# Kernel optimization log

Measured on AMD Instinct MI355X. Metric: run time of the kernel, lower is better.

The kernel has to match this reference:

```python
import jax, jax.numpy as jnp
import numpy as np

C_IMG, C_TXT, NHEAD = 256, 768, 8
B, D, H, W, L = 8, 24, 24, 24, 77

def setup_inputs() -> dict:
    key = jax.random.key(0)
    ks = jax.random.split(key, 16)
    s = 0.02
    x_img = jax.random.normal(ks[0], (B, C_IMG, D, H, W), jnp.float32)
    x_txt = jax.random.normal(ks[1], (B, L, C_TXT), jnp.float32)
    # realistic padding: each sample has a valid length in [40, 77); True = padded key
    lengths = jax.random.randint(ks[2], (B,), 40, L)
    txt_mask = jnp.arange(L)[None, :] >= lengths[:, None]  # [B, L] bool
    inp = {
        "x_img": x_img,
        "x_txt": x_txt,
        "txt_mask": txt_mask,
        "q_proj_w": jax.random.normal(ks[3], (C_IMG, C_IMG), jnp.float32) * s,   # Conv3d 1x1, no bias
        "k_proj_w": jax.random.normal(ks[4], (C_IMG, C_TXT), jnp.float32) * s,   # Linear, no bias
        "v_proj_w": jax.random.normal(ks[5], (C_IMG, C_TXT), jnp.float32) * s,
        "in_q_w": jax.random.normal(ks[6], (C_IMG, C_IMG), jnp.float32) * s,     # MHA in_proj (q/k/v)
        "in_q_b": jnp.zeros((C_IMG,), jnp.float32),
        "in_k_w": jax.random.normal(ks[7], (C_IMG, C_IMG), jnp.float32) * s,
        "in_k_b": jnp.zeros((C_IMG,), jnp.float32),
        "in_v_w": jax.random.normal(ks[8], (C_IMG, C_IMG), jnp.float32) * s,
        "in_v_b": jnp.zeros((C_IMG,), jnp.float32),
        "out_proj_w": jax.random.normal(ks[9], (C_IMG, C_IMG), jnp.float32) * s, # MHA out_proj
        "out_proj_b": jnp.zeros((C_IMG,), jnp.float32),
        "out_conv_w": jax.random.normal(ks[10], (C_IMG, C_IMG), jnp.float32) * s, # self.out Conv3d 1x1 (bias)
        "out_conv_b": jnp.zeros((C_IMG,), jnp.float32),
        "norm_w": jnp.ones((C_IMG,), jnp.float32),  # InstanceNorm3d affine
        "norm_b": jnp.zeros((C_IMG,), jnp.float32),
    }
    return inp

def reference(x_img, x_txt, txt_mask, q_proj_w, k_proj_w, v_proj_w,
              in_q_w, in_q_b, in_k_w, in_k_b, in_v_w, in_v_b,
              out_proj_w, out_proj_b, out_conv_w, out_conv_b, norm_w, norm_b):
    Bq, C, d, h, w = x_img.shape
    N = d * h * w
    hd = C // NHEAD
    # q_proj (1x1 conv == channel matmul), flatten to tokens
    q = jnp.einsum('bcdhw,oc->bodhw', x_img, q_proj_w).reshape(Bq, C, N).transpose(0, 2, 1)  # [B,N,C]
    k = jnp.einsum('blt,ct->blc', x_txt, k_proj_w)  # [B,L,C]
    v = jnp.einsum('blt,ct->blc', x_txt, v_proj_w)
    # MHA internal projections
    qh = (q @ in_q_w.T + in_q_b).reshape(Bq, N, NHEAD, hd).transpose(0, 2, 1, 3)  # [B,h,N,hd]
    kh = (k @ in_k_w.T + in_k_b).reshape(Bq, -1, NHEAD, hd).transpose(0, 2, 1, 3)  # [B,h,L,hd]
    vh = (v @ in_v_w.T + in_v_b).reshape(Bq, -1, NHEAD, hd).transpose(0, 2, 1, 3)
    scores = jnp.einsum('bhnd,bhld->bhnl', qh, kh) / jnp.sqrt(jnp.asarray(hd, qh.dtype))
    neg = jnp.finfo(scores.dtype).min
    scores = jnp.where(txt_mask[:, None, None, :], neg, scores)
    attn = jax.nn.softmax(scores, axis=-1)  # [B,h,N,L]
    o = jnp.einsum('bhnl,bhld->bhnd', attn, vh).transpose(0, 2, 1, 3).reshape(Bq, N, C)
    o = o @ out_proj_w.T + out_proj_b
    o = o.transpose(0, 2, 1).reshape(Bq, C, d, h, w)
    # self.out 1x1 conv with bias
    o = jnp.einsum('bcdhw,oc->bodhw', o, out_conv_w) + out_conv_b[None, :, None, None, None]
    # residual + InstanceNorm3d(affine) + SiLU
    r = o + x_img
    mu = r.mean(axis=(2, 3, 4), keepdims=True)
    var = r.var(axis=(2, 3, 4), keepdims=True)
    xn = (r - mu) * jax.lax.rsqrt(var + 1e-5)
    out = jax.nn.silu(xn * norm_w[None, :, None, None, None] + norm_b[None, :, None, None, None])
    return out
```

## Files before the change

### kernel.cpp

```cpp
#include <hip/hip_runtime.h>
#include <cstdint>
#include <cstddef>

#define B_    8
#define CI    256
#define NH    8
#define HD    32
#define LQ    77
#define LP    80
#define NSP   13824
#define NTILE 216
#define SCALE 0.17677669529663687f

typedef float    float4_ __attribute__((ext_vector_type(4)));
typedef _Float16 half4_  __attribute__((ext_vector_type(4)));

#define MFMA16(a,b,c) __builtin_amdgcn_mfma_f32_16x16x16f16((a),(b),(c),0,0,0)

#define OFF_WK   0
#define OFF_WV   (OFF_WK + 256*768)
#define OFF_BO   (OFF_WV + 256*768)
#define OFF_IQBS (OFF_BO + 256)
#define OFF_AM   (OFF_IQBS + 256)
#define OFF_WQP  (OFF_AM + B_*LP)
#define OFF_WOP  (OFF_WQP + 32768)
#define OFF_KP   (OFF_WOP + 32768)
#define OFF_VP   (OFF_KP + 81920)

__global__ __launch_bounds__(256) void prep_kernel(
    const float* __restrict__ qpw, const float* __restrict__ iqw,
    const float* __restrict__ opw, const float* __restrict__ opb,
    const float* __restrict__ ocw, const float* __restrict__ ocb,
    const float* __restrict__ kpw, const float* __restrict__ ikw,
    const float* __restrict__ vpw, const float* __restrict__ ivw,
    const float* __restrict__ iqb,
    const void*  __restrict__ mask_in, float* __restrict__ ws)
{
    int blk = blockIdx.x, tid = threadIdx.x;
    if (blk < 512) {
        __shared__ float col[256];
        int cc = blk & 255;
        bool isQ = blk < 256;
        const float* pw = isQ ? qpw : opw;
        const float* iw = isQ ? iqw : ocw;
        col[tid] = pw[tid * 256 + cc];
        __syncthreads();
        const float* row = iw + tid * 256;
        float a = 0.f;
        #pragma unroll 4
        for (int m = 0; m < 256; ++m) a = fmaf(row[m], col[m], a);
        if (isQ) a *= SCALE;
        _Float16* dst = (_Float16*)(ws + (isQ ? OFF_WQP : OFF_WOP));
        int kt = cc >> 4, ot = tid >> 4;
        int lane = (tid & 15) + 16 * ((cc >> 2) & 3);
        dst[((kt * 16 + ot) * 64 + lane) * 4 + (cc & 3)] = (_Float16)a;
    } else if (blk == 512) {
        float a = ocb[tid];
        const float* row = ocw + tid * 256;
        #pragma unroll 4
        for (int m = 0; m < 256; ++m) a = fmaf(row[m], opb[m], a);
        ws[OFF_BO + tid] = a;
        ws[OFF_IQBS + tid] = iqb[tid] * SCALE;
    } else if (blk < 513 + 2 * 768) {
        int j = blk - 513;
        bool isK = j < 768;
        if (!isK) j -= 768;
        int flat = j * 256 + tid;
        int o = flat / 768, tt = flat % 768;
        const float* iw = isK ? ikw : ivw;
        const float* pw = isK ? kpw : vpw;
        const float* row = iw + o * 256;
        float a = 0.f;
        #pragma unroll 4
        for (int m = 0; m < 256; ++m) a = fmaf(row[m], pw[m * 768 + tt], a);
        ws[(isK ? OFF_WK : OFF_WV) + flat] = a;
    } else {
        __shared__ int s_is8;
        if (tid == 0) s_is8 = 0;
        __syncthreads();
        const unsigned char* m8 = (const unsigned char*)mask_in;
        for (int i = tid; i < B_ * LQ; i += 256)
            if ((i & 3) && m8[i]) atomicExch(&s_is8, 1);
        __syncthreads();
        int is8 = s_is8;
        const int* mi = (const int*)mask_in;
        float* mo = ws + OFF_AM;
        for (int i = tid; i < B_ * LP; i += 256) {
            int b = i / LP, l = i % LP;
            int v = 1;
            if (l < LQ) v = is8 ? (int)m8[b * LQ + l] : mi[b * LQ + l];
            mo[i] = v ? -1e30f : 0.0f;
        }
    }
}

__global__ __launch_bounds__(256) void kv_kernel(
    const float* __restrict__ xtxt, float* __restrict__ ws,
    const float* __restrict__ ikb, const float* __restrict__ ivb)
{
    const float* Wk = ws + OFF_WK;
    const float* Wv = ws + OFF_WV;
    _Float16* kp = (_Float16*)(ws + OFF_KP);
    _Float16* vp = (_Float16*)(ws + OFF_VP);

    int b = blockIdx.y;
    int l0 = blockIdx.x * 8;
    int lcnt = (LQ - l0 < 8) ? (LQ - l0) : 8;
    __shared__ float xr[8][768];
    for (int idx = threadIdx.x; idx < 8 * 768; idx += 256) {
        int j = idx / 768, tt = idx % 768;
        xr[j][tt] = (j < lcnt) ? xtxt[((size_t)(b * LQ + l0 + j)) * 768 + tt] : 0.f;
    }
    __syncthreads();
    int o = threadIdx.x;
    float ak[8], av[8];
    #pragma unroll
    for (int j = 0; j < 8; ++j) { ak[j] = ikb[o]; av[j] = ivb[o]; }
    const float* wkr = Wk + (size_t)o * 768;
    const float* wvr = Wv + (size_t)o * 768;
    for (int tt = 0; tt < 768; ++tt) {
        float wk = wkr[tt], wv = wvr[tt];
        #pragma unroll
        for (int j = 0; j < 8; ++j) {
            ak[j] = fmaf(wk, xr[j][tt], ak[j]);
            av[j] = fmaf(wv, xr[j][tt], av[j]);
        }
    }
    int h = o >> 5, d = o & 31;
    size_t hb = (size_t)(b * NH + h);
    #pragma unroll
    for (int j = 0; j < 8; ++j) {
        if (j < lcnt) {
            int l = l0 + j;
            int lt = l >> 4;
            kp[(hb * 10 + lt * 2 + (d >> 4)) * 256 +
               ((l & 15) + 16 * ((d >> 2) & 3)) * 4 + (d & 3)] = (_Float16)ak[j];
            vp[(hb * 10 + (d >> 4) * 5 + lt) * 256 +
               ((d & 15) + 16 * ((l & 15) >> 2)) * 4 + (l & 3)] = (_Float16)av[j];
        }
    }
}

__global__ __launch_bounds__(256, 2) void main_kernel(
    const float* __restrict__ x_img, const float* __restrict__ ws,
    float* __restrict__ rout)
{
    const _Float16* wqpk = (const _Float16*)(ws + OFF_WQP);
    const _Float16* wopk = (const _Float16*)(ws + OFF_WOP);
    const _Float16* kpck = (const _Float16*)(ws + OFF_KP);
    const _Float16* vpck = (const _Float16*)(ws + OFF_VP);
    const float* iqbs = ws + OFF_IQBS;
    const float* bog  = ws + OFF_BO;

    __shared__ _Float16 sh0[16384];
    __shared__ _Float16 qls[16384];
    __shared__ float am_s[LP];

    const int tid  = threadIdx.x;
    const int lane = tid & 63;
    const int w    = __builtin_amdgcn_readfirstlane(tid >> 6);
    const int g    = lane >> 4;
    const int li   = lane & 15;
    const int by   = blockIdx.y;
    const int n0   = blockIdx.x * 64;

    const float* xba = x_img + (size_t)by * CI * NSP + n0;
    float*       rba = rout  + (size_t)by * CI * NSP + n0;

    if (tid < LP) am_s[tid] = ws[OFF_AM + by * LP + tid];

    for (int it = 0; it < 8; ++it) {
        int idx = it * 256 + tid;
        int c = idx >> 3, hl = idx & 7;
        const float* gp = xba + (size_t)c * NSP + hl * 8;
        float4_ a = *(const float4_*)gp;
        float4_ bvv = *(const float4_*)(gp + 4);
        int kt = c >> 4;
        int lhi = 16 * ((c >> 2) & 3);
        int jj = c & 3;
        #pragma unroll
        for (int u = 0; u < 8; ++u) {
            int t = hl * 8 + u;
            float v = (u < 4) ? a[u] : bvv[u - 4];
            sh0[((kt * 4 + (t >> 4)) * 64 + (t & 15) + lhi) * 4 + jj] = (_Float16)v;
        }
    }
    __syncthreads();

    float4_ acc[4][4];
    #pragma unroll
    for (int of = 0; of < 4; ++of) {
        float bs[4];
        #pragma unroll
        for (int r = 0; r < 4; ++r) bs[r] = iqbs[w * 64 + of * 16 + 4 * g + r];
        #pragma unroll
        for (int tf = 0; tf < 4; ++tf)
            #pragma unroll
            for (int r = 0; r < 4; ++r) acc[of][tf][r] = bs[r];
    }
    for (int kt = 0; kt < 16; ++kt) {
        half4_ bfr[4], afr[4];
        #pragma unroll
        for (int tf = 0; tf < 4; ++tf)
            bfr[tf] = *(const half4_*)&sh0[((kt * 4 + tf) * 64 + lane) * 4];
        #pragma unroll
        for (int of = 0; of < 4; ++of)
            afr[of] = *(const half4_*)&wqpk[((kt * 16 + w * 4 + of) * 64 + lane) * 4];
        #pragma unroll
        for (int of = 0; of < 4; ++of)
            #pragma unroll
            for (int tf = 0; tf < 4; ++tf)
                acc[of][tf] = MFMA16(afr[of], bfr[tf], acc[of][tf]);
    }
    #pragma unroll
    for (int of = 0; of < 4; ++of)
        #pragma unroll
        for (int tf = 0; tf < 4; ++tf) {
            half4_ qv;
            #pragma unroll
            for (int r = 0; r < 4; ++r) qv[r] = (_Float16)acc[of][tf][r];
            *(half4_*)&qls[((( w * 4 + of) * 4 + tf) * 64 + lane) * 4] = qv;
        }
    __syncthreads();

    for (int hh = 0; hh < 2; ++hh) {
        const int h = 2 * w + hh;
        half4_ qb[2][4];
        #pragma unroll
        for (int kd = 0; kd < 2; ++kd)
            #pragma unroll
            for (int tf = 0; tf < 4; ++tf)
                qb[kd][tf] = *(const half4_*)&qls[(((h * 2 + kd) * 4 + tf) * 64 + lane) * 4];
        float4_ sc[5][4];
        #pragma unroll
        for (int lt = 0; lt < 5; ++lt)
            #pragma unroll
            for (int tf = 0; tf < 4; ++tf)
                #pragma unroll
                for (int r = 0; r < 4; ++r) sc[lt][tf][r] = 0.f;
        const _Float16* kp = kpck + (size_t)(by * NH + h) * 10 * 256;
        #pragma unroll
        for (int lt = 0; lt < 5; ++lt)
            #pragma unroll
            for (int kd = 0; kd < 2; ++kd) {
                half4_ akf = *(const half4_*)&kp[((lt * 2 + kd) * 64 + lane) * 4];
                #pragma unroll
                for (int tf = 0; tf < 4; ++tf)
                    sc[lt][tf] = MFMA16(akf, qb[kd][tf], sc[lt][tf]);
            }
        float mk[5][4];
        #pragma unroll
        for (int lt = 0; lt < 5; ++lt)
            #pragma unroll
            for (int r = 0; r < 4; ++r) mk[lt][r] = am_s[lt * 16 + 4 * g + r];
        #pragma unroll
        for (int lt = 0; lt < 5; ++lt)
            #pragma unroll
            for (int tf = 0; tf < 4; ++tf)
                #pragma unroll
                for (int r = 0; r < 4; ++r) sc[lt][tf][r] += mk[lt][r];
        float mx[4], sm[4], inv[4];
        #pragma unroll
        for (int tf = 0; tf < 4; ++tf) {
            float m = -3.0e38f;
            #pragma unroll
            for (int lt = 0; lt < 5; ++lt)
                #pragma unroll
                for (int r = 0; r < 4; ++r) m = fmaxf(m, sc[lt][tf][r]);
            m = fmaxf(m, __shfl_xor(m, 16));
            m = fmaxf(m, __shfl_xor(m, 32));
            mx[tf] = m;
        }
        #pragma unroll
        for (int tf = 0; tf < 4; ++tf) {
            float s = 0.f;
            #pragma unroll
            for (int lt = 0; lt < 5; ++lt)
                #pragma unroll
                for (int r = 0; r < 4; ++r) {
                    float e = __expf(sc[lt][tf][r] - mx[tf]);
                    sc[lt][tf][r] = e;
                    s += e;
                }
            s += __shfl_xor(s, 16);
            s += __shfl_xor(s, 32);
            sm[tf] = s;
            inv[tf] = 1.0f / s;
        }
        float4_ oa[2][4];
        #pragma unroll
        for (int dt = 0; dt < 2; ++dt)
            #pragma unroll
            for (int tf = 0; tf < 4; ++tf)
                #pragma unroll
                for (int r = 0; r < 4; ++r) oa[dt][tf][r] = 0.f;
        const _Float16* vp = vpck + (size_t)(by * NH + h) * 10 * 256;
        #pragma unroll
        for (int lt = 0; lt < 5; ++lt) {
            half4_ pl[4];
            #pragma unroll
            for (int tf = 0; tf < 4; ++tf) {
                #pragma unroll
                for (int r = 0; r < 4; ++r) pl[tf][r] = (_Float16)sc[lt][tf][r];
            }
            #pragma unroll
            for (int dt = 0; dt < 2; ++dt) {
                half4_ avf = *(const half4_*)&vp[((dt * 5 + lt) * 64 + lane) * 4];
                #pragma unroll
                for (int tf = 0; tf < 4; ++tf)
                    oa[dt][tf] = MFMA16(avf, pl[tf], oa[dt][tf]);
            }
        }
        #pragma unroll
        for (int dt = 0; dt < 2; ++dt)
            #pragma unroll
            for (int tf = 0; tf < 4; ++tf) {
                half4_ ov;
                #pragma unroll
                for (int r = 0; r < 4; ++r) ov[r] = (_Float16)(oa[dt][tf][r] * inv[tf]);
                *(half4_*)&sh0[(((h * 2 + dt) * 4 + tf) * 64 + lane) * 4] = ov;
            }
    }
    __syncthreads();

    float4_ fa[4][4];
    #pragma unroll
    for (int of = 0; of < 4; ++of) {
        float bs[4];
        #pragma unroll
        for (int r = 0; r < 4; ++r) bs[r] = bog[w * 64 + of * 16 + 4 * g + r];
        #pragma unroll
        for (int tf = 0; tf < 4; ++tf)
            #pragma unroll
            for (int r = 0; r < 4; ++r) fa[of][tf][r] = bs[r];
    }
    for (int kt = 0; kt < 16; ++kt) {
        half4_ bfr[4], afr[4];
        #pragma unroll
        for (int tf = 0; tf < 4; ++tf)
            bfr[tf] = *(const half4_*)&sh0[((kt * 4 + tf) * 64 + lane) * 4];
        #pragma unroll
        for (int of = 0; of < 4; ++of)
            afr[of] = *(const half4_*)&wopk[((kt * 16 + w * 4 + of) * 64 + lane) * 4];
        #pragma unroll
        for (int of = 0; of < 4; ++of)
            #pragma unroll
            for (int tf = 0; tf < 4; ++tf)
                fa[of][tf] = MFMA16(afr[of], bfr[tf], fa[of][tf]);
    }
    #pragma unroll
    for (int of = 0; of < 4; ++of)
        #pragma unroll
        for (int tf = 0; tf < 4; ++tf)
            #pragma unroll
            for (int r = 0; r < 4; ++r) {
                int o = w * 64 + of * 16 + 4 * g + r;
                int t = tf * 16 + li;
                size_t a = (size_t)o * NSP + t;
                rba[a] = fa[of][tf][r] + xba[a];
            }
}

__global__ __launch_bounds__(256) void norm_kernel(
    float* __restrict__ rout, const float* __restrict__ nw, const float* __restrict__ nb)
{
    __shared__ float red[8];
    __shared__ float stats[2];
    int blk = blockIdx.x;
    int c = blk & 255;
    float* row = rout + (size_t)blk * NSP;
    float4_* row4 = (float4_*)row;
    int tid = threadIdx.x;

    float s = 0.f, s2 = 0.f;
    for (int i = tid; i < NSP / 4; i += 256) {
        float4_ v = row4[i];
        #pragma unroll
        for (int u = 0; u < 4; ++u) { s += v[u]; s2 = fmaf(v[u], v[u], s2); }
    }
    #pragma unroll
    for (int off = 32; off > 0; off >>= 1) {
        s  += __shfl_down(s, off);
        s2 += __shfl_down(s2, off);
    }
    int wv = tid >> 6, ln = tid & 63;
    if (ln == 0) { red[wv] = s; red[4 + wv] = s2; }
    __syncthreads();
    if (tid == 0) {
        float S  = red[0] + red[1] + red[2] + red[3];
        float S2 = red[4] + red[5] + red[6] + red[7];
        float mu = S / (float)NSP;
        float var = S2 / (float)NSP - mu * mu;
        stats[0] = mu;
        stats[1] = rsqrtf(var + 1e-5f);
    }
    __syncthreads();
    float mu = stats[0], rstd = stats[1];
    float gg  = nw[c] * rstd;
    float b2 = fmaf(-mu, gg, nb[c]);
    for (int i = tid; i < NSP / 4; i += 256) {
        float4_ v = row4[i];
        #pragma unroll
        for (int u = 0; u < 4; ++u) {
            float y = fmaf(v[u], gg, b2);
            v[u] = y / (1.f + __expf(-y));
        }
        row4[i] = v;
    }
}

extern "C" void kernel_launch(void* const* d_in, const int* in_sizes, int n_in,
                              void* d_out, int out_size, void* d_ws, size_t ws_size,
                              hipStream_t stream) {
    const float* x_img = (const float*)d_in[0];
    const float* x_txt = (const float*)d_in[1];
    const void*  tmask = d_in[2];
    const float* qpw   = (const float*)d_in[3];
    const float* kpw   = (const float*)d_in[4];
    const float* vpw   = (const float*)d_in[5];
    const float* iqw   = (const float*)d_in[6];
    const float* iqb   = (const float*)d_in[7];
    const float* ikw   = (const float*)d_in[8];
    const float* ikb   = (const float*)d_in[9];
    const float* ivw   = (const float*)d_in[10];
    const float* ivb   = (const float*)d_in[11];
    const float* opw   = (const float*)d_in[12];
    const float* opb   = (const float*)d_in[13];
    const float* ocw   = (const float*)d_in[14];
    const float* ocb   = (const float*)d_in[15];
    const float* nw    = (const float*)d_in[16];
    const float* nb    = (const float*)d_in[17];
    float* ws  = (float*)d_ws;
    float* out = (float*)d_out;

    prep_kernel<<<2050, 256, 0, stream>>>(qpw, iqw, opw, opb, ocw, ocb,
                                          kpw, ikw, vpw, ivw, iqb, tmask, ws);
    kv_kernel<<<dim3(10, B_), 256, 0, stream>>>(x_txt, ws, ikb, ivb);
    main_kernel<<<dim3(NTILE, B_), 256, 0, stream>>>(x_img, ws, out);
    norm_kernel<<<B_ * CI, 256, 0, stream>>>(out, nw, nb);
}
```

Baseline: 513.5 us.

## Move weight combining and KV projection to MFMA, fuse norm stats into main kernel

The scalar weight-combination and K/V projection kernels are replaced with MFMA-based fp16 versions that write directly into the packed fragment layouts. The main kernel drops the second shared buffer to raise occupancy to 3 blocks per CU. It also stages its output through swizzled shared memory for coalesced stores and accumulates per-channel sum and sum-of-squares with atomics. The norm kernel then only reads the precomputed stats and does a single pass over the data instead of two. The cost is extra fp16 rounding of weights and inputs, plus atomic contention on the statistics buffer.

```diff
diff --git a/kernel.cpp b/kernel.cpp
--- a/kernel.cpp
+++ b/kernel.cpp
@@ -17,64 +17,31 @@
 
 #define MFMA16(a,b,c) __builtin_amdgcn_mfma_f32_16x16x16f16((a),(b),(c),0,0,0)
 
-#define OFF_WK   0
-#define OFF_WV   (OFF_WK + 256*768)
-#define OFF_BO   (OFF_WV + 256*768)
-#define OFF_IQBS (OFF_BO + 256)
-#define OFF_AM   (OFF_IQBS + 256)
-#define OFF_WQP  (OFF_AM + B_*LP)
-#define OFF_WOP  (OFF_WQP + 32768)
-#define OFF_KP   (OFF_WOP + 32768)
-#define OFF_VP   (OFF_KP + 81920)
+#define OFF_WQP  0
+#define OFF_WOP  32768
+#define OFF_WKP  65536
+#define OFF_WVP  163840
+#define OFF_KP   262144
+#define OFF_VP   344064
+#define OFF_BO   425984
+#define OFF_IQBS 426240
+#define OFF_AM   426496
+#define OFF_STAT 427136
 
 __global__ __launch_bounds__(256) void prep_kernel(
-    const float* __restrict__ qpw, const float* __restrict__ iqw,
-    const float* __restrict__ opw, const float* __restrict__ opb,
-    const float* __restrict__ ocw, const float* __restrict__ ocb,
-    const float* __restrict__ kpw, const float* __restrict__ ikw,
-    const float* __restrict__ vpw, const float* __restrict__ ivw,
-    const float* __restrict__ iqb,
+    const float* __restrict__ opb, const float* __restrict__ ocw,
+    const float* __restrict__ ocb, const float* __restrict__ iqb,
     const void*  __restrict__ mask_in, float* __restrict__ ws)
 {
     int blk = blockIdx.x, tid = threadIdx.x;
-    if (blk < 512) {
-        __shared__ float col[256];
-        int cc = blk & 255;
-        bool isQ = blk < 256;
-        const float* pw = isQ ? qpw : opw;
-        const float* iw = isQ ? iqw : ocw;
-        col[tid] = pw[tid * 256 + cc];
-        __syncthreads();
-        const float* row = iw + tid * 256;
-        float a = 0.f;
-        #pragma unroll 4
-        for (int m = 0; m < 256; ++m) a = fmaf(row[m], col[m], a);
-        if (isQ) a *= SCALE;
-        _Float16* dst = (_Float16*)(ws + (isQ ? OFF_WQP : OFF_WOP));
-        int kt = cc >> 4, ot = tid >> 4;
-        int lane = (tid & 15) + 16 * ((cc >> 2) & 3);
-        dst[((kt * 16 + ot) * 64 + lane) * 4 + (cc & 3)] = (_Float16)a;
-    } else if (blk == 512) {
+    if (blk == 0) {
         float a = ocb[tid];
         const float* row = ocw + tid * 256;
         #pragma unroll 4
         for (int m = 0; m < 256; ++m) a = fmaf(row[m], opb[m], a);
         ws[OFF_BO + tid] = a;
         ws[OFF_IQBS + tid] = iqb[tid] * SCALE;
-    } else if (blk < 513 + 2 * 768) {
-        int j = blk - 513;
-        bool isK = j < 768;
-        if (!isK) j -= 768;
-        int flat = j * 256 + tid;
-        int o = flat / 768, tt = flat % 768;
-        const float* iw = isK ? ikw : ivw;
-        const float* pw = isK ? kpw : vpw;
-        const float* row = iw + o * 256;
-        float a = 0.f;
-        #pragma unroll 4
-        for (int m = 0; m < 256; ++m) a = fmaf(row[m], pw[m * 768 + tt], a);
-        ws[(isK ? OFF_WK : OFF_WV) + flat] = a;
-    } else {
+    } else if (blk == 1) {
         __shared__ int s_is8;
         if (tid == 0) s_is8 = 0;
         __syncthreads();
@@ -91,6 +58,67 @@
             if (l < LQ) v = is8 ? (int)m8[b * LQ + l] : mi[b * LQ + l];
             mo[i] = v ? -1e30f : 0.0f;
         }
+    } else {
+        for (int i = tid; i < B_ * CI * 2; i += 256) ws[OFF_STAT + i] = 0.f;
+    }
+}
+
+__global__ __launch_bounds__(256) void wcomb_kernel(
+    const float* __restrict__ qpw, const float* __restrict__ iqw,
+    const float* __restrict__ opw, const float* __restrict__ ocw,
+    const float* __restrict__ kpw, const float* __restrict__ ikw,
+    const float* __restrict__ vpw, const float* __restrict__ ivw,
+    float* __restrict__ ws)
+{
+    int blk = blockIdx.x, tid = threadIdx.x;
+    int lane = tid & 63, w = tid >> 6, g = lane >> 4, li = lane & 15;
+
+    const float *iw, *pw; _Float16* dst; int pstride, ctb, otb; float scale = 1.f;
+    if (blk < 16) {
+        iw = iqw; pw = qpw; pstride = 256; dst = (_Float16*)(ws + OFF_WQP);
+        ctb = blk >> 2; otb = blk & 3; scale = SCALE;
+    } else if (blk < 32) {
+        int j = blk - 16;
+        iw = ocw; pw = opw; pstride = 256; dst = (_Float16*)(ws + OFF_WOP);
+        ctb = j >> 2; otb = j & 3;
+    } else if (blk < 80) {
+        int j = blk - 32;
+        iw = ikw; pw = kpw; pstride = 768; dst = (_Float16*)(ws + OFF_WKP);
+        ctb = j >> 2; otb = j & 3;
+    } else {
+        int j = blk - 80;
+        iw = ivw; pw = vpw; pstride = 768; dst = (_Float16*)(ws + OFF_WVP);
+        ctb = j >> 2; otb = j & 3;
+    }
+    int ct = ctb * 4 + w;
+
+    float4_ acc[4];
+    #pragma unroll
+    for (int i = 0; i < 4; ++i)
+        #pragma unroll
+        for (int r = 0; r < 4; ++r) acc[i][r] = 0.f;
+
+    for (int mt = 0; mt < 16; ++mt) {
+        half4_ ah;
+        #pragma unroll
+        for (int j = 0; j < 4; ++j)
+            ah[j] = (_Float16)pw[(size_t)(mt * 16 + 4 * g + j) * pstride + ct * 16 + li];
+        #pragma unroll
+        for (int i = 0; i < 4; ++i) {
+            int o = (otb * 4 + i) * 16 + li;
+            float4_ bw = *(const float4_*)&iw[(size_t)o * 256 + mt * 16 + 4 * g];
+            half4_ bh;
+            #pragma unroll
+            for (int j = 0; j < 4; ++j) bh[j] = (_Float16)bw[j];
+            acc[i] = MFMA16(ah, bh, acc[i]);
+        }
+    }
+    #pragma unroll
+    for (int i = 0; i < 4; ++i) {
+        half4_ oh;
+        #pragma unroll
+        for (int r = 0; r < 4; ++r) oh[r] = (_Float16)(acc[i][r] * scale);
+        *(half4_*)&dst[((size_t)(ct * 16 + otb * 4 + i) * 64 + lane) * 4] = oh;
     }
 }
 
@@ -98,52 +126,86 @@
     const float* __restrict__ xtxt, float* __restrict__ ws,
     const float* __restrict__ ikb, const float* __restrict__ ivb)
 {
-    const float* Wk = ws + OFF_WK;
-    const float* Wv = ws + OFF_WV;
+    const _Float16* wkA = (const _Float16*)(ws + OFF_WKP);
+    const _Float16* wvA = (const _Float16*)(ws + OFF_WVP);
     _Float16* kp = (_Float16*)(ws + OFF_KP);
     _Float16* vp = (_Float16*)(ws + OFF_VP);
 
-    int b = blockIdx.y;
-    int l0 = blockIdx.x * 8;
-    int lcnt = (LQ - l0 < 8) ? (LQ - l0) : 8;
-    __shared__ float xr[8][768];
-    for (int idx = threadIdx.x; idx < 8 * 768; idx += 256) {
-        int j = idx / 768, tt = idx % 768;
-        xr[j][tt] = (j < lcnt) ? xtxt[((size_t)(b * LQ + l0 + j)) * 768 + tt] : 0.f;
-    }
-    __syncthreads();
-    int o = threadIdx.x;
-    float ak[8], av[8];
-    #pragma unroll
-    for (int j = 0; j < 8; ++j) { ak[j] = ikb[o]; av[j] = ivb[o]; }
-    const float* wkr = Wk + (size_t)o * 768;
-    const float* wvr = Wv + (size_t)o * 768;
-    for (int tt = 0; tt < 768; ++tt) {
-        float wk = wkr[tt], wv = wvr[tt];
-        #pragma unroll
-        for (int j = 0; j < 8; ++j) {
-            ak[j] = fmaf(wk, xr[j][tt], ak[j]);
-            av[j] = fmaf(wv, xr[j][tt], av[j]);
-        }
-    }
-    int h = o >> 5, d = o & 31;
-    size_t hb = (size_t)(b * NH + h);
-    #pragma unroll
-    for (int j = 0; j < 8; ++j) {
-        if (j < lcnt) {
-            int l = l0 + j;
-            int lt = l >> 4;
-            kp[(hb * 10 + lt * 2 + (d >> 4)) * 256 +
-               ((l & 15) + 16 * ((d >> 2) & 3)) * 4 + (d & 3)] = (_Float16)ak[j];
-            vp[(hb * 10 + (d >> 4) * 5 + lt) * 256 +
-               ((d & 15) + 16 * ((l & 15) >> 2)) * 4 + (l & 3)] = (_Float16)av[j];
-        }
-    }
-}
-
-__global__ __launch_bounds__(256, 2) void main_kernel(
+    int b = blockIdx.x >> 1, part = blockIdx.x & 1;
+    int tid = threadIdx.x, lane = tid & 63, w = tid >> 6, g = lane >> 4, li = lane & 15;
+
+    float4_ acc[4][5];
+    if (part == 0) {
+        #pragma unroll
+        for (int i = 0; i < 4; ++i) {
+            float4_ bias = *(const float4_*)&ikb[(w * 4 + i) * 16 + 4 * g];
+            #pragma unroll
+            for (int lt = 0; lt < 5; ++lt) acc[i][lt] = bias;
+        }
+    } else {
+        #pragma unroll
+        for (int i = 0; i < 4; ++i) {
+            float bv = ivb[(w * 4 + i) * 16 + li];
+            #pragma unroll
+            for (int lt = 0; lt < 5; ++lt)
+                #pragma unroll
+                for (int r = 0; r < 4; ++r) acc[i][lt][r] = bv;
+        }
+    }
+
+    for (int kt = 0; kt < 48; ++kt) {
+        half4_ xh[5];
+        #pragma unroll
+        for (int lt = 0; lt < 5; ++lt) {
+            int l = lt * 16 + li;
+            float4_ xv = {0.f, 0.f, 0.f, 0.f};
+            if (l < LQ)
+                xv = *(const float4_*)&xtxt[(size_t)(b * LQ + l) * 768 + kt * 16 + 4 * g];
+            #pragma unroll
+            for (int j = 0; j < 4; ++j) xh[lt][j] = (_Float16)xv[j];
+        }
+        if (part == 0) {
+            #pragma unroll
+            for (int i = 0; i < 4; ++i) {
+                half4_ aw = *(const half4_*)&wkA[((size_t)(kt * 16 + w * 4 + i) * 64 + lane) * 4];
+                #pragma unroll
+                for (int lt = 0; lt < 5; ++lt)
+                    acc[i][lt] = MFMA16(aw, xh[lt], acc[i][lt]);
+            }
+        } else {
+            #pragma unroll
+            for (int i = 0; i < 4; ++i) {
+                half4_ bw = *(const half4_*)&wvA[((size_t)(kt * 16 + w * 4 + i) * 64 + lane) * 4];
+                #pragma unroll
+                for (int lt = 0; lt < 5; ++lt)
+                    acc[i][lt] = MFMA16(xh[lt], bw, acc[i][lt]);
+            }
+        }
+    }
+
+    #pragma unroll
+    for (int i = 0; i < 4; ++i) {
+        int ot = w * 4 + i, h = ot >> 1;
+        size_t hb = (size_t)(b * NH + h) * 10;
+        #pragma unroll
+        for (int lt = 0; lt < 5; ++lt) {
+            half4_ oh;
+            #pragma unroll
+            for (int r = 0; r < 4; ++r) oh[r] = (_Float16)acc[i][lt][r];
+            if (part == 0) {
+                int kd = ot & 1;
+                *(half4_*)&kp[(hb + lt * 2 + kd) * 256 + lane * 4] = oh;
+            } else {
+                int dt = ot & 1;
+                *(half4_*)&vp[(hb + dt * 5 + lt) * 256 + lane * 4] = oh;
+            }
+        }
+    }
+}
+
+__global__ __launch_bounds__(256, 3) void main_kernel(
     const float* __restrict__ x_img, const float* __restrict__ ws,
-    float* __restrict__ rout)
+    float* __restrict__ rout, float* __restrict__ stat)
 {
     const _Float16* wqpk = (const _Float16*)(ws + OFF_WQP);
     const _Float16* wopk = (const _Float16*)(ws + OFF_WOP);
@@ -153,7 +215,6 @@
     const float* bog  = ws + OFF_BO;
 
     __shared__ _Float16 sh0[16384];
-    __shared__ _Float16 qls[16384];
     __shared__ float am_s[LP];
 
     const int tid  = threadIdx.x;
@@ -169,34 +230,150 @@
 
     if (tid < LP) am_s[tid] = ws[OFF_AM + by * LP + tid];
 
-    for (int it = 0; it < 8; ++it) {
-        int idx = it * 256 + tid;
-        int c = idx >> 3, hl = idx & 7;
-        const float* gp = xba + (size_t)c * NSP + hl * 8;
-        float4_ a = *(const float4_*)gp;
-        float4_ bvv = *(const float4_*)(gp + 4);
-        int kt = c >> 4;
-        int lhi = 16 * ((c >> 2) & 3);
-        int jj = c & 3;
-        #pragma unroll
-        for (int u = 0; u < 8; ++u) {
-            int t = hl * 8 + u;
-            float v = (u < 4) ? a[u] : bvv[u - 4];
-            sh0[((kt * 4 + (t >> 4)) * 64 + (t & 15) + lhi) * 4 + jj] = (_Float16)v;
+    {
+        int t = tid & 63, tf_s = t >> 4, tl = t & 15;
+        for (int it = 0; it < 16; ++it) {
+            int cbase = it * 16 + 4 * w;
+            half4_ hv;
+            #pragma unroll
+            for (int j = 0; j < 4; ++j)
+                hv[j] = (_Float16)xba[(size_t)(cbase + j) * NSP + t];
+            *(half4_*)&sh0[((it * 4 + tf_s) * 64 + tl + 16 * w) * 4] = hv;
         }
     }
     __syncthreads();
 
-    float4_ acc[4][4];
+    half4_ qh_h[4][4];
+    {
+        float4_ acc[4][4];
+        #pragma unroll
+        for (int of = 0; of < 4; ++of) {
+            float4_ bias = *(const float4_*)&iqbs[w * 64 + of * 16 + 4 * g];
+            #pragma unroll
+            for (int tf = 0; tf < 4; ++tf) acc[of][tf] = bias;
+        }
+        for (int kt = 0; kt < 16; ++kt) {
+            half4_ bfr[4], afr[4];
+            #pragma unroll
+            for (int tf = 0; tf < 4; ++tf)
+                bfr[tf] = *(const half4_*)&sh0[((kt * 4 + tf) * 64 + lane) * 4];
+            #pragma unroll
+            for (int of = 0; of < 4; ++of)
+                afr[of] = *(const half4_*)&wqpk[((size_t)(kt * 16 + w * 4 + of) * 64 + lane) * 4];
+            #pragma unroll
+            for (int of = 0; of < 4; ++of)
+                #pragma unroll
+                for (int tf = 0; tf < 4; ++tf)
+                    acc[of][tf] = MFMA16(afr[of], bfr[tf], acc[of][tf]);
+        }
+        #pragma unroll
+        for (int of = 0; of < 4; ++of)
+            #pragma unroll
+            for (int tf = 0; tf < 4; ++tf)
+                #pragma unroll
+                for (int r = 0; r < 4; ++r)
+                    qh_h[of][tf][r] = (_Float16)acc[of][tf][r];
+    }
+    __syncthreads();
+
+    #pragma unroll
+    for (int hh = 0; hh < 2; ++hh) {
+        const int h = 2 * w + hh;
+        const _Float16* kp = kpck + (size_t)(by * NH + h) * 2560;
+        const _Float16* vp = vpck + (size_t)(by * NH + h) * 2560;
+        float mk[5][4];
+        #pragma unroll
+        for (int lt = 0; lt < 5; ++lt)
+            #pragma unroll
+            for (int r = 0; r < 4; ++r) mk[lt][r] = am_s[lt * 16 + 4 * g + r];
+        #pragma unroll
+        for (int tfh = 0; tfh < 2; ++tfh) {
+            float4_ sc[5][2];
+            #pragma unroll
+            for (int lt = 0; lt < 5; ++lt)
+                #pragma unroll
+                for (int t2 = 0; t2 < 2; ++t2)
+                    #pragma unroll
+                    for (int r = 0; r < 4; ++r) sc[lt][t2][r] = 0.f;
+            #pragma unroll
+            for (int lt = 0; lt < 5; ++lt)
+                #pragma unroll
+                for (int kd = 0; kd < 2; ++kd) {
+                    half4_ akf = *(const half4_*)&kp[((lt * 2 + kd) * 64 + lane) * 4];
+                    #pragma unroll
+                    for (int t2 = 0; t2 < 2; ++t2)
+                        sc[lt][t2] = MFMA16(akf, qh_h[2 * hh + kd][tfh * 2 + t2], sc[lt][t2]);
+                }
+            #pragma unroll
+            for (int lt = 0; lt < 5; ++lt)
+                #pragma unroll
+                for (int t2 = 0; t2 < 2; ++t2)
+                    #pragma unroll
+                    for (int r = 0; r < 4; ++r) sc[lt][t2][r] += mk[lt][r];
+            float inv[2];
+            #pragma unroll
+            for (int t2 = 0; t2 < 2; ++t2) {
+                float m = -3.0e38f;
+                #pragma unroll
+                for (int lt = 0; lt < 5; ++lt)
+                    #pragma unroll
+                    for (int r = 0; r < 4; ++r) m = fmaxf(m, sc[lt][t2][r]);
+                m = fmaxf(m, __shfl_xor(m, 16));
+                m = fmaxf(m, __shfl_xor(m, 32));
+                float s = 0.f;
+                #pragma unroll
+                for (int lt = 0; lt < 5; ++lt)
+                    #pragma unroll
+                    for (int r = 0; r < 4; ++r) {
+                        float e = __expf(sc[lt][t2][r] - m);
+                        sc[lt][t2][r] = e;
+                        s += e;
+                    }
+                s += __shfl_xor(s, 16);
+                s += __shfl_xor(s, 32);
+                inv[t2] = 1.0f / s;
+            }
+            float4_ oa[2][2];
+            #pragma unroll
+            for (int dt = 0; dt < 2; ++dt)
+                #pragma unroll
+                for (int t2 = 0; t2 < 2; ++t2)
+                    #pragma unroll
+                    for (int r = 0; r < 4; ++r) oa[dt][t2][r] = 0.f;
+            #pragma unroll
+            for (int lt = 0; lt < 5; ++lt) {
+                half4_ pl[2];
+                #pragma unroll
+                for (int t2 = 0; t2 < 2; ++t2)
+                    #pragma unroll
+                    for (int r = 0; r < 4; ++r) pl[t2][r] = (_Float16)sc[lt][t2][r];
+                #pragma unroll
+                for (int dt = 0; dt < 2; ++dt) {
+                    half4_ avf = *(const half4_*)&vp[((dt * 5 + lt) * 64 + lane) * 4];
+                    #pragma unroll
+                    for (int t2 = 0; t2 < 2; ++t2)
+                        oa[dt][t2] = MFMA16(avf, pl[t2], oa[dt][t2]);
+                }
+            }
+            #pragma unroll
+            for (int dt = 0; dt < 2; ++dt)
+                #pragma unroll
+                for (int t2 = 0; t2 < 2; ++t2) {
+                    half4_ ov;
+                    #pragma unroll
+                    for (int r = 0; r < 4; ++r) ov[r] = (_Float16)(oa[dt][t2][r] * inv[t2]);
+                    *(half4_*)&sh0[(((h * 2 + dt) * 4 + tfh * 2 + t2) * 64 + lane) * 4] = ov;
+                }
+        }
+    }
+    __syncthreads();
+
+    float4_ fa[4][4];
     #pragma unroll
     for (int of = 0; of < 4; ++of) {
-        float bs[4];
-        #pragma unroll
-        for (int r = 0; r < 4; ++r) bs[r] = iqbs[w * 64 + of * 16 + 4 * g + r];
-        #pragma unroll
-        for (int tf = 0; tf < 4; ++tf)
-            #pragma unroll
-            for (int r = 0; r < 4; ++r) acc[of][tf][r] = bs[r];
+        float4_ bias = *(const float4_*)&bog[w * 64 + of * 16 + 4 * g];
+        #pragma unroll
+        for (int tf = 0; tf < 4; ++tf) fa[of][tf] = bias;
     }
     for (int kt = 0; kt < 16; ++kt) {
         half4_ bfr[4], afr[4];
@@ -205,200 +382,69 @@
             bfr[tf] = *(const half4_*)&sh0[((kt * 4 + tf) * 64 + lane) * 4];
         #pragma unroll
         for (int of = 0; of < 4; ++of)
-            afr[of] = *(const half4_*)&wqpk[((kt * 16 + w * 4 + of) * 64 + lane) * 4];
-        #pragma unroll
-        for (int of = 0; of < 4; ++of)
-            #pragma unroll
-            for (int tf = 0; tf < 4; ++tf)
-                acc[of][tf] = MFMA16(afr[of], bfr[tf], acc[of][tf]);
-    }
-    #pragma unroll
-    for (int of = 0; of < 4; ++of)
-        #pragma unroll
-        for (int tf = 0; tf < 4; ++tf) {
-            half4_ qv;
-            #pragma unroll
-            for (int r = 0; r < 4; ++r) qv[r] = (_Float16)acc[of][tf][r];
-            *(half4_*)&qls[((( w * 4 + of) * 4 + tf) * 64 + lane) * 4] = qv;
-        }
-    __syncthreads();
-
-    for (int hh = 0; hh < 2; ++hh) {
-        const int h = 2 * w + hh;
-        half4_ qb[2][4];
-        #pragma unroll
-        for (int kd = 0; kd < 2; ++kd)
-            #pragma unroll
-            for (int tf = 0; tf < 4; ++tf)
-                qb[kd][tf] = *(const half4_*)&qls[(((h * 2 + kd) * 4 + tf) * 64 + lane) * 4];
-        float4_ sc[5][4];
-        #pragma unroll
-        for (int lt = 0; lt < 5; ++lt)
-            #pragma unroll
-            for (int tf = 0; tf < 4; ++tf)
-                #pragma unroll
-                for (int r = 0; r < 4; ++r) sc[lt][tf][r] = 0.f;
-        const _Float16* kp = kpck + (size_t)(by * NH + h) * 10 * 256;
-        #pragma unroll
-        for (int lt = 0; lt < 5; ++lt)
-            #pragma unroll
-            for (int kd = 0; kd < 2; ++kd) {
-                half4_ akf = *(const half4_*)&kp[((lt * 2 + kd) * 64 + lane) * 4];
-                #pragma unroll
-                for (int tf = 0; tf < 4; ++tf)
-                    sc[lt][tf] = MFMA16(akf, qb[kd][tf], sc[lt][tf]);
-            }
-        float mk[5][4];
-        #pragma unroll
-        for (int lt = 0; lt < 5; ++lt)
-            #pragma unroll
-            for (int r = 0; r < 4; ++r) mk[lt][r] = am_s[lt * 16 + 4 * g + r];
-        #pragma unroll
-        for (int lt = 0; lt < 5; ++lt)
-            #pragma unroll
-            for (int tf = 0; tf < 4; ++tf)
-                #pragma unroll
-                for (int r = 0; r < 4; ++r) sc[lt][tf][r] += mk[lt][r];
-        float mx[4], sm[4], inv[4];
-        #pragma unroll
-        for (int tf = 0; tf < 4; ++tf) {
-            float m = -3.0e38f;
-            #pragma unroll
-            for (int lt = 0; lt < 5; ++lt)
-                #pragma unroll
-                for (int r = 0; r < 4; ++r) m = fmaxf(m, sc[lt][tf][r]);
-            m = fmaxf(m, __shfl_xor(m, 16));
-            m = fmaxf(m, __shfl_xor(m, 32));
-            mx[tf] = m;
-        }
-        #pragma unroll
-        for (int tf = 0; tf < 4; ++tf) {
-            float s = 0.f;
-            #pragma unroll
-            for (int lt = 0; lt < 5; ++lt)
-                #pragma unroll
-                for (int r = 0; r < 4; ++r) {
-                    float e = __expf(sc[lt][tf][r] - mx[tf]);
-                    sc[lt][tf][r] = e;
-                    s += e;
-                }
-            s += __shfl_xor(s, 16);
-            s += __shfl_xor(s, 32);
-            sm[tf] = s;
-            inv[tf] = 1.0f / s;
-        }
-        float4_ oa[2][4];
-        #pragma unroll
-        for (int dt = 0; dt < 2; ++dt)
-            #pragma unroll
-            for (int tf = 0; tf < 4; ++tf)
-                #pragma unroll
-                for (int r = 0; r < 4; ++r) oa[dt][tf][r] = 0.f;
-        const _Float16* vp = vpck + (size_t)(by * NH + h) * 10 * 256;
-        #pragma unroll
-        for (int lt = 0; lt < 5; ++lt) {
-            half4_ pl[4];
-            #pragma unroll
-            for (int tf = 0; tf < 4; ++tf) {
-                #pragma unroll
-                for (int r = 0; r < 4; ++r) pl[tf][r] = (_Float16)sc[lt][tf][r];
-            }
-            #pragma unroll
-            for (int dt = 0; dt < 2; ++dt) {
-                half4_ avf = *(const half4_*)&vp[((dt * 5 + lt) * 64 + lane) * 4];
-                #pragma unroll
-                for (int tf = 0; tf < 4; ++tf)
-                    oa[dt][tf] = MFMA16(avf, pl[tf], oa[dt][tf]);
-            }
-        }
-        #pragma unroll
-        for (int dt = 0; dt < 2; ++dt)
-            #pragma unroll
-            for (int tf = 0; tf < 4; ++tf) {
-                half4_ ov;
-                #pragma unroll
-                for (int r = 0; r < 4; ++r) ov[r] = (_Float16)(oa[dt][tf][r] * inv[tf]);
-                *(half4_*)&sh0[(((h * 2 + dt) * 4 + tf) * 64 + lane) * 4] = ov;
-            }
-    }
-    __syncthreads();
-
-    float4_ fa[4][4];
-    #pragma unroll
-    for (int of = 0; of < 4; ++of) {
-        float bs[4];
-        #pragma unroll
-        for (int r = 0; r < 4; ++r) bs[r] = bog[w * 64 + of * 16 + 4 * g + r];
-        #pragma unroll
-        for (int tf = 0; tf < 4; ++tf)
-            #pragma unroll
-            for (int r = 0; r < 4; ++r) fa[of][tf][r] = bs[r];
-    }
-    for (int kt = 0; kt < 16; ++kt) {
-        half4_ bfr[4], afr[4];
-        #pragma unroll
-        for (int tf = 0; tf < 4; ++tf)
-            bfr[tf] = *(const half4_*)&sh0[((kt * 4 + tf) * 64 + lane) * 4];
-        #pragma unroll
-        for (int of = 0; of < 4; ++of)
-            afr[of] = *(const half4_*)&wopk[((kt * 16 + w * 4 + of) * 64 + lane) * 4];
+            afr[of] = *(const half4_*)&wopk[((size_t)(kt * 16 + w * 4 + of) * 64 + lane) * 4];
         #pragma unroll
         for (int of = 0; of < 4; ++of)
             #pragma unroll
             for (int tf = 0; tf < 4; ++tf)
                 fa[of][tf] = MFMA16(afr[of], bfr[tf], fa[of][tf]);
     }
+    __syncthreads();
+
     #pragma unroll
     for (int of = 0; of < 4; ++of)
         #pragma unroll
         for (int tf = 0; tf < 4; ++tf)
             #pragma unroll
             for (int r = 0; r < 4; ++r) {
-                int o = w * 64 + of * 16 + 4 * g + r;
-                int t = tf * 16 + li;
-                size_t a = (size_t)o * NSP + t;
-                rba[a] = fa[of][tf][r] + xba[a];
-            }
+                int row = w * 64 + of * 16 + 4 * g + r;
+                int q   = tf * 4 + (li >> 2);
+                int qs  = q ^ (4 * g + r);
+                sh0[row * 64 + qs * 4 + (li & 3)] = (_Float16)fa[of][tf][r];
+            }
+    __syncthreads();
+
+    for (int it = 0; it < 16; ++it) {
+        int flat = it * 256 + tid;
+        int row = flat >> 4, q = flat & 15;
+        half4_ hv = *(const half4_*)&sh0[row * 64 + ((q ^ (row & 15)) << 2)];
+        float4_ xres = *(const float4_*)&xba[(size_t)row * NSP + q * 4];
+        float4_ y;
+        float s = 0.f, s2 = 0.f;
+        #pragma unroll
+        for (int e = 0; e < 4; ++e) {
+            y[e] = (float)hv[e] + xres[e];
+            s += y[e];
+            s2 = fmaf(y[e], y[e], s2);
+        }
+        *(float4_*)&rba[(size_t)row * NSP + q * 4] = y;
+        #pragma unroll
+        for (int off = 1; off < 16; off <<= 1) {
+            s  += __shfl_xor(s, off);
+            s2 += __shfl_xor(s2, off);
+        }
+        if ((tid & 15) == 0) {
+            atomicAdd(&stat[(by * CI + row) * 2],     s);
+            atomicAdd(&stat[(by * CI + row) * 2 + 1], s2);
+        }
+    }
 }
 
 __global__ __launch_bounds__(256) void norm_kernel(
-    float* __restrict__ rout, const float* __restrict__ nw, const float* __restrict__ nb)
+    float* __restrict__ rout, const float* __restrict__ nw,
+    const float* __restrict__ nb, const float* __restrict__ stat)
 {
-    __shared__ float red[8];
-    __shared__ float stats[2];
     int blk = blockIdx.x;
     int c = blk & 255;
-    float* row = rout + (size_t)blk * NSP;
-    float4_* row4 = (float4_*)row;
-    int tid = threadIdx.x;
-
-    float s = 0.f, s2 = 0.f;
-    for (int i = tid; i < NSP / 4; i += 256) {
-        float4_ v = row4[i];
-        #pragma unroll
-        for (int u = 0; u < 4; ++u) { s += v[u]; s2 = fmaf(v[u], v[u], s2); }
-    }
-    #pragma unroll
-    for (int off = 32; off > 0; off >>= 1) {
-        s  += __shfl_down(s, off);
-        s2 += __shfl_down(s2, off);
-    }
-    int wv = tid >> 6, ln = tid & 63;
-    if (ln == 0) { red[wv] = s; red[4 + wv] = s2; }
-    __syncthreads();
-    if (tid == 0) {
-        float S  = red[0] + red[1] + red[2] + red[3];
-        float S2 = red[4] + red[5] + red[6] + red[7];
-        float mu = S / (float)NSP;
-        float var = S2 / (float)NSP - mu * mu;
-        stats[0] = mu;
-        stats[1] = rsqrtf(var + 1e-5f);
-    }
-    __syncthreads();
-    float mu = stats[0], rstd = stats[1];
-    float gg  = nw[c] * rstd;
+    float S  = stat[blk * 2];
+    float S2 = stat[blk * 2 + 1];
+    float mu = S * (1.0f / (float)NSP);
+    float var = S2 * (1.0f / (float)NSP) - mu * mu;
+    float rstd = rsqrtf(var + 1e-5f);
+    float gg = nw[c] * rstd;
     float b2 = fmaf(-mu, gg, nb[c]);
-    for (int i = tid; i < NSP / 4; i += 256) {
+    float4_* row4 = (float4_*)(rout + (size_t)blk * NSP);
+    for (int i = threadIdx.x; i < NSP / 4; i += 256) {
         float4_ v = row4[i];
         #pragma unroll
         for (int u = 0; u < 4; ++u) {
@@ -433,9 +479,9 @@
     float* ws  = (float*)d_ws;
     float* out = (float*)d_out;
 
-    prep_kernel<<<2050, 256, 0, stream>>>(qpw, iqw, opw, opb, ocw, ocb,
-                                          kpw, ikw, vpw, ivw, iqb, tmask, ws);
-    kv_kernel<<<dim3(10, B_), 256, 0, stream>>>(x_txt, ws, ikb, ivb);
-    main_kernel<<<dim3(NTILE, B_), 256, 0, stream>>>(x_img, ws, out);
-    norm_kernel<<<B_ * CI, 256, 0, stream>>>(out, nw, nb);
-}
+    prep_kernel<<<3, 256, 0, stream>>>(opb, ocw, ocb, iqb, tmask, ws);
+    wcomb_kernel<<<128, 256, 0, stream>>>(qpw, iqw, opw, ocw, kpw, ikw, vpw, ivw, ws);
+    kv_kernel<<<16, 256, 0, stream>>>(x_txt, ws, ikb, ivb);
+    main_kernel<<<dim3(NTILE, B_), 256, 0, stream>>>(x_img, ws, out, ws + OFF_STAT);
+    norm_kernel<<<B_ * CI, 256, 0, stream>>>(out, nw, nb, ws + OFF_STAT);
+}
```

Result: no change. 504.6 us (-1.7%).
